# Kernel optimization log

Hardware: AMD Instinct MI355X
Metric: run time of the kernel (lower is better)

Reference implementation:

```python
import jax, jax.numpy as jnp
import numpy as np

NUM_HEADS = 12


def setup_inputs() -> dict:
    key = jax.random.key(0)
    k_x, k_m, k_qkv, k_proj = jax.random.split(key, 4)
    B, N, C = 2, 2048, 768
    x = jax.random.normal(k_x, (B, N, C), dtype=jnp.float32)
    # binary key mask: 1 = attend, 0 = masked out
    mask = jax.random.randint(k_m, (B, N), 0, 2).astype(jnp.int32)
    # torch Linear(dim, dim*3, bias=False): stored here as [in, out]
    w_qkv = jax.random.normal(k_qkv, (C, 3 * C), dtype=jnp.float32) * 0.02
    w_proj = jax.random.normal(k_proj, (C, C), dtype=jnp.float32) * 0.02
    b_proj = jnp.zeros((C,), dtype=jnp.float32)
    return {"x": x, "mask": mask, "w_qkv": w_qkv, "w_proj": w_proj, "b_proj": b_proj}


def reference(x, mask, w_qkv, w_proj, b_proj):
    B, N, C = x.shape
    H = NUM_HEADS
    hd = C // H
    scale = hd ** -0.5
    qkv = (x @ w_qkv).reshape(B, N, 3, H, hd)
    q, k, v = jnp.moveaxis(qkv, 2, 0)            # each [B, N, H, hd]
    attn = jnp.einsum('bnhd,bmhd->bhnm', q, k) * scale  # [B, H, N, N]
    # faithful masked_softmax: unstable exp (no max subtraction), mask keys, renormalize
    m = mask.astype(x.dtype)[:, None, None, :]   # [B, 1, 1, N]
    x_exp = jnp.exp(attn) * m
    attn = x_exp / x_exp.sum(-1, keepdims=True)
    out = jnp.einsum('bhnm,bmhd->bnhd', attn, v).reshape(B, N, C)
    return out @ w_proj + b_proj
```

## Files before the change

kernel.cpp:

```cpp
#include <hip/hip_runtime.h>
#include <cstdint>

#define NB 2
#define NSEQ 2048
#define CDIM 768
#define NH 12
#define HD 64
#define NTOK (NB*NSEQ)
#define QKV_COLS (3*CDIM)
#define NBLK ((NSEQ/64)*NH*NB)

typedef short bf16x8 __attribute__((ext_vector_type(8)));
typedef short bf16x4 __attribute__((ext_vector_type(4)));
typedef float f32x4  __attribute__((ext_vector_type(4)));
typedef short short4v __attribute__((ext_vector_type(4)));
typedef unsigned int uint4v __attribute__((ext_vector_type(4)));

#define MFMA16(a,b,c) __builtin_amdgcn_mfma_f32_16x16x32_bf16(a,b,c,0,0,0)

__device__ __forceinline__ short f2b(float f) {
    uint32_t u = __builtin_bit_cast(uint32_t, f);
    u += 0x7fffu + ((u >> 16) & 1u);
    return (short)(u >> 16);
}
__device__ __forceinline__ unsigned pack2(float a, float b) {
    unsigned ua = __builtin_bit_cast(unsigned, a) + 0x7fffu;
    unsigned ub = __builtin_bit_cast(unsigned, b) + 0x7fffu;
    return __builtin_amdgcn_perm(ub, ua, 0x07060302u);
}
__device__ __forceinline__ void gll16(const short* g, short* l) {
    __builtin_amdgcn_global_load_lds(
        (const __attribute__((address_space(1))) unsigned int*)g,
        (__attribute__((address_space(3))) unsigned int*)l, 16, 0, 0);
}

__global__ __launch_bounds__(256) void prep_kernel(
    const float* __restrict__ x, const float* __restrict__ w_qkv,
    const float* __restrict__ w_proj,
    short* __restrict__ xb, short* __restrict__ wqt, short* __restrict__ wpt)
{
    __shared__ float tile[32][33];
    const int bid = blockIdx.x, t = threadIdx.x;
    if (bid < 3072) {
        int i = bid * 256 + t;
        float4 v = ((const float4*)x)[i];
        short4v o = { f2b(v.x), f2b(v.y), f2b(v.z), f2b(v.w) };
        ((short4v*)xb)[i] = o;
        return;
    }
    const float* w; short* wt; int K, NC, n0, k0;
    if (bid < 3072 + 1728) {
        int r = bid - 3072;
        w = w_qkv; wt = wqt; K = CDIM; NC = QKV_COLS;
        n0 = (r % 72) * 32; k0 = (r / 72) * 32;
    } else {
        int r = bid - 4800;
        w = w_proj; wt = wpt; K = CDIM; NC = CDIM;
        n0 = (r % 24) * 32; k0 = (r / 24) * 32;
    }
    #pragma unroll
    for (int i = 0; i < 4; ++i) {
        int idx = t + i * 256; int r = idx >> 5, c = idx & 31;
        tile[r][c] = w[(size_t)(k0 + r) * NC + n0 + c];
    }
    __syncthreads();
    #pragma unroll
    for (int i = 0; i < 4; ++i) {
        int idx = t + i * 256; int r = idx >> 5, c = idx & 31;
        wt[(size_t)(n0 + r) * K + k0 + c] = f2b(tile[c][r]);
    }
}

__global__ __launch_bounds__(256) void gemm_qkv(
    const short* __restrict__ A ,
    const short* __restrict__ B ,
    short* __restrict__ qb, short* __restrict__ kb, short* __restrict__ vt)
{
    __shared__ short As[128 * 32];
    __shared__ short Bs[128 * 32];
    const int t = threadIdx.x;
    const int lane = t & 63, wid = t >> 6;
    const int quad = lane >> 4, l16 = lane & 15;
    const int wA = wid >> 1, wB = wid & 1;
    const int n0 = blockIdx.x * 128;
    const int m0 = blockIdx.y * 128;

    const int srow = wid * 16 + (lane >> 2), schunk = (lane & 3) * 8;
    const short* ag0 = A + (size_t)(n0 + srow) * CDIM + schunk;
    const short* ag1 = ag0 + (size_t)64 * CDIM;
    const short* bg0 = B + (size_t)(m0 + srow) * CDIM + schunk;
    const short* bg1 = bg0 + (size_t)64 * CDIM;
    short* asl0 = &As[(wid * 16) * 32];
    short* asl1 = &As[(wid * 16 + 64) * 32];
    short* bsl0 = &Bs[(wid * 16) * 32];
    short* bsl1 = &Bs[(wid * 16 + 64) * 32];

    f32x4 acc[4][4] = {};
    for (int k0 = 0; k0 < CDIM; k0 += 32) {
        __syncthreads();
        gll16(ag0 + k0, asl0);
        gll16(ag1 + k0, asl1);
        gll16(bg0 + k0, bsl0);
        gll16(bg1 + k0, bsl1);
        __syncthreads();
        bf16x8 af[4], bf[4];
        #pragma unroll
        for (int i = 0; i < 4; ++i)
            af[i] = *(const bf16x8*)&As[(wA*64 + i*16 + l16) * 32 + quad*8];
        #pragma unroll
        for (int j = 0; j < 4; ++j)
            bf[j] = *(const bf16x8*)&Bs[(wB*64 + j*16 + l16) * 32 + quad*8];
        #pragma unroll
        for (int i = 0; i < 4; ++i)
            #pragma unroll
            for (int j = 0; j < 4; ++j)
                acc[i][j] = MFMA16(af[i], bf[j], acc[i][j]);
    }

    const int colbase = n0 + wA * 64;
    const int s = colbase / CDIM;
    const int h = (colbase - s * CDIM) >> 6;
    const int b = m0 >> 11;
    const size_t bh = (size_t)(b * NH + h);
    const float qsc = (s == 0) ? 0.125f : 1.0f;
    #pragma unroll
    for (int i = 0; i < 4; ++i) {
        const int d0 = i*16 + quad*4;
        #pragma unroll
        for (int j = 0; j < 4; ++j) {
            int tok = (m0 + wB*64 + j*16 + l16) & (NSEQ - 1);
            if (s < 2) {
                short* dst = (s == 0 ? qb : kb) + (bh * NSEQ + tok) * HD + d0;
                short4v o = { f2b(acc[i][j][0] * qsc), f2b(acc[i][j][1] * qsc),
                              f2b(acc[i][j][2] * qsc), f2b(acc[i][j][3] * qsc) };
                *(short4v*)dst = o;
            } else {
                short* dst = vt + (bh * HD + d0) * NSEQ + tok;
                #pragma unroll
                for (int r = 0; r < 4; ++r)
                    dst[(size_t)r * NSEQ] = f2b(acc[i][j][r]);
            }
        }
    }
}

#define STAGE(KT, BUF) do {                                                      \
    short* kb_ = (BUF);                                                          \
    short* vb_ = (BUF) + 8192;                                                   \
    _Pragma("unroll")                                                            \
    for (int j = 0; j < 4; ++j) {                                                \
        gll16(kp + (size_t)((KT) + rK[j]) * HD + cK[j]*8,                        \
              kb_ + wid*2048 + j*512);                                           \
        gll16(vp + (size_t)dV[j] * NSEQ + (KT) + cV[j]*8,                        \
              vb_ + wid*2048 + j*512);                                           \
    }                                                                            \
} while (0)

#define BODY(KT, BUF) do {                                                       \
    const short* KsB_ = (BUF);                                                   \
    const short* VsB_ = (BUF) + 8192;                                            \
    int4 mi0_ = *(const int4*)(mp + (KT) + kbase);                               \
    int4 mi1_ = *(const int4*)(mp + (KT) + 64 + kbase);                          \
    bf16x8 kf00_ = *(const bf16x8*)&KsB_[krow + kc0];                            \
    bf16x8 kf01_ = *(const bf16x8*)&KsB_[krow + kc1];                            \
    bf16x8 kf10_ = *(const bf16x8*)&KsB_[4096 + krow + kc0];                     \
    bf16x8 kf11_ = *(const bf16x8*)&KsB_[4096 + krow + kc1];                     \
    f32x4 s0_[4] = {}, s1_[4] = {};                                              \
    _Pragma("unroll")                                                            \
    for (int jt = 0; jt < 4; ++jt) {                                             \
        s0_[jt] = MFMA16(kf00_, qf[jt][0], s0_[jt]);                             \
        s0_[jt] = MFMA16(kf01_, qf[jt][1], s0_[jt]);                             \
        s1_[jt] = MFMA16(kf10_, qf[jt][0], s1_[jt]);                             \
        s1_[jt] = MFMA16(kf11_, qf[jt][1], s1_[jt]);                             \
    }                                                                            \
    float4 m0_ = {(float)mi0_.x, (float)mi0_.y, (float)mi0_.z, (float)mi0_.w};   \
    float4 m1_ = {(float)mi1_.x, (float)mi1_.y, (float)mi1_.z, (float)mi1_.w};   \
    bf16x8 pb_[4];                                                               \
    _Pragma("unroll")                                                            \
    for (int jt = 0; jt < 4; ++jt) {                                             \
        float e0 = __expf(s0_[jt][0]) * m0_.x;                                   \
        float e1 = __expf(s0_[jt][1]) * m0_.y;                                   \
        float e2 = __expf(s0_[jt][2]) * m0_.z;                                   \
        float e3 = __expf(s0_[jt][3]) * m0_.w;                                   \
        float f0 = __expf(s1_[jt][0]) * m1_.x;                                   \
        float f1 = __expf(s1_[jt][1]) * m1_.y;                                   \
        float f2 = __expf(s1_[jt][2]) * m1_.z;                                   \
        float f3 = __expf(s1_[jt][3]) * m1_.w;                                   \
        l[jt] += ((e0 + e1) + (e2 + e3)) + ((f0 + f1) + (f2 + f3));              \
        uint4v pk_ = { pack2(e0, e1), pack2(e2, e3),                             \
                       pack2(f0, f1), pack2(f2, f3) };                           \
        pb_[jt] = __builtin_bit_cast(bf16x8, pk_);                               \
    }                                                                            \
    _Pragma("unroll")                                                            \
    for (int it = 0; it < 4; ++it) {                                             \
        const int vrow_ = (it*16 + l16) * 128;                                   \
        bf16x4 lo_ = *(const bf16x4*)&VsB_[vrow_ + vposl + vsub];                \
        bf16x4 hi_ = *(const bf16x4*)&VsB_[vrow_ + vposh + vsub];                \
        bf16x8 vf_ = __builtin_shufflevector(lo_, hi_, 0,1,2,3,4,5,6,7);         \
        _Pragma("unroll")                                                        \
        for (int jt = 0; jt < 4; ++jt)                                           \
            o_acc[it][jt] = MFMA16(vf_, pb_[jt], o_acc[it][jt]);                 \
    }                                                                            \
} while (0)

__global__ __launch_bounds__(256, 2) void attn_kernel(
    const short* __restrict__ qb, const short* __restrict__ kb,
    const short* __restrict__ vt, const int* __restrict__ mask,
    short* __restrict__ ao)
{
    __shared__ __align__(16) short KV[2][16384];
    float (*Ob)[68] = (float(*)[68])KV;
    float (*lsum)[64] = (float(*)[64])((char*)KV + 17408);

    const int t = threadIdx.x;
    const int lane = t & 63, wid = t >> 6;
    const int quad = lane >> 4, l16 = lane & 15;
    const int id = blockIdx.x;
    const int idx = id >> 3;
    const int bh = (id & 7) + ((idx % 3) << 3);
    const int q0 = (idx / 3) << 6;
    const int b = bh / NH, h = bh - b * NH;
    const size_t hoff = (size_t)bh * NSEQ * HD;
    const short* qp = qb + hoff;
    const short* kp = kb + hoff;
    const short* vp = vt + hoff;
    const int* mp = mask + b * NSEQ;
    const int kbase = wid * 16 + quad * 4;

    int rK[4], cK[4], dV[4], cV[4];
    #pragma unroll
    for (int j = 0; j < 4; ++j) {
        int o = wid * 4096 + j * 1024 + lane * 16;
        rK[j] = o >> 7;
        cK[j] = ((o >> 4) & 7) ^ (rK[j] & 7);
        dV[j] = o >> 8;
        cV[j] = ((o >> 4) & 15) ^ (dV[j] & 15);
    }
    const int r7 = l16 & 7;
    const int krow = (wid * 16 + l16) * 64;
    const int kc0 = ((quad     ^ r7) << 3);
    const int kc1 = (((quad+4) ^ r7) << 3);
    const int vposl = ((wid*2 + (quad >> 1)) ^ l16) << 3;
    const int vposh = (((8 + wid*2 + (quad >> 1)) ^ l16) << 3);
    const int vsub = (quad & 1) * 4;

    bf16x8 qf[4][2];
    #pragma unroll
    for (int jt = 0; jt < 4; ++jt) {
        const short* qr = qp + (size_t)(q0 + jt*16 + l16) * HD + quad*8;
        qf[jt][0] = *(const bf16x8*)qr;
        qf[jt][1] = *(const bf16x8*)(qr + 32);
    }

    f32x4 o_acc[4][4] = {};
    float l[4] = {0.f, 0.f, 0.f, 0.f};

    STAGE(0, KV[0]);
    __syncthreads();

    for (int kt = 0; kt < NSEQ; kt += 256) {
        STAGE(kt + 128, KV[1]);
        BODY(kt, KV[0]);
        __syncthreads();
        const int nx = (kt + 256) & (NSEQ - 1);
        STAGE(nx, KV[0]);
        BODY(kt + 128, KV[1]);
        __syncthreads();
    }

    #pragma unroll
    for (int jt = 0; jt < 4; ++jt) {
        l[jt] += __shfl_xor(l[jt], 16);
        l[jt] += __shfl_xor(l[jt], 32);
        if (quad == 0) lsum[wid][jt*16 + l16] = l[jt];
    }
    for (int w = 0; w < 4; ++w) {
        __syncthreads();
        if (wid == w) {
            #pragma unroll
            for (int it = 0; it < 4; ++it)
                #pragma unroll
                for (int jt = 0; jt < 4; ++jt)
                    #pragma unroll
                    for (int r = 0; r < 4; ++r) {
                        if (w == 0)
                            Ob[it*16 + quad*4 + r][jt*16 + l16] = o_acc[it][jt][r];
                        else
                            Ob[it*16 + quad*4 + r][jt*16 + l16] += o_acc[it][jt][r];
                    }
        }
    }
    __syncthreads();

    {
        const int ql = t >> 2, dc = (t & 3) * 16;
        float inv = 1.0f / (((lsum[0][ql] + lsum[1][ql]) +
                             (lsum[2][ql] + lsum[3][ql])));
        bf16x8 o8a, o8b;
        #pragma unroll
        for (int d = 0; d < 8; ++d) o8a[d] = f2b(Ob[dc + d][ql] * inv);
        #pragma unroll
        for (int d = 0; d < 8; ++d) o8b[d] = f2b(Ob[dc + 8 + d][ql] * inv);
        int tok = b * NSEQ + q0 + ql;
        short* dst = ao + (size_t)tok * CDIM + h * HD + dc;
        *(bf16x8*)dst = o8a;
        *(bf16x8*)(dst + 8) = o8b;
    }
}

__global__ __launch_bounds__(256) void gemm_proj(
    const short* __restrict__ A ,
    const short* __restrict__ B ,
    const float* __restrict__ bias, float* __restrict__ out)
{
    __shared__ short As[128 * 32];
    __shared__ short Bs[128 * 32];
    const int t = threadIdx.x;
    const int lane = t & 63, wid = t >> 6;
    const int quad = lane >> 4, l16 = lane & 15;
    const int wA = wid >> 1, wB = wid & 1;
    const int n0 = blockIdx.x * 128;
    const int m0 = blockIdx.y * 128;

    const int srow = wid * 16 + (lane >> 2), schunk = (lane & 3) * 8;
    const short* ag0 = A + (size_t)(n0 + srow) * CDIM + schunk;
    const short* ag1 = ag0 + (size_t)64 * CDIM;
    const short* bg0 = B + (size_t)(m0 + srow) * CDIM + schunk;
    const short* bg1 = bg0 + (size_t)64 * CDIM;
    short* asl0 = &As[(wid * 16) * 32];
    short* asl1 = &As[(wid * 16 + 64) * 32];
    short* bsl0 = &Bs[(wid * 16) * 32];
    short* bsl1 = &Bs[(wid * 16 + 64) * 32];

    f32x4 acc[4][4] = {};
    for (int k0 = 0; k0 < CDIM; k0 += 32) {
        __syncthreads();
        gll16(ag0 + k0, asl0);
        gll16(ag1 + k0, asl1);
        gll16(bg0 + k0, bsl0);
        gll16(bg1 + k0, bsl1);
        __syncthreads();
        bf16x8 af[4], bf[4];
        #pragma unroll
        for (int i = 0; i < 4; ++i)
            af[i] = *(const bf16x8*)&As[(wA*64 + i*16 + l16) * 32 + quad*8];
        #pragma unroll
        for (int j = 0; j < 4; ++j)
            bf[j] = *(const bf16x8*)&Bs[(wB*64 + j*16 + l16) * 32 + quad*8];
        #pragma unroll
        for (int i = 0; i < 4; ++i)
            #pragma unroll
            for (int j = 0; j < 4; ++j)
                acc[i][j] = MFMA16(af[i], bf[j], acc[i][j]);
    }

    #pragma unroll
    for (int i = 0; i < 4; ++i) {
        int col0 = n0 + wA*64 + i*16 + quad*4;
        float4 bias4 = *(const float4*)&bias[col0];
        #pragma unroll
        for (int j = 0; j < 4; ++j) {
            int tok = m0 + wB*64 + j*16 + l16;
            float4 o = { acc[i][j][0] + bias4.x, acc[i][j][1] + bias4.y,
                         acc[i][j][2] + bias4.z, acc[i][j][3] + bias4.w };
            *(float4*)(out + (size_t)tok * CDIM + col0) = o;
        }
    }
}

extern "C" void kernel_launch(void* const* d_in, const int* in_sizes, int n_in,
                              void* d_out, int out_size, void* d_ws, size_t ws_size,
                              hipStream_t stream)
{
    const float* x      = (const float*)d_in[0];
    const int*   mask   = (const int*)d_in[1];
    const float* w_qkv  = (const float*)d_in[2];
    const float* w_proj = (const float*)d_in[3];
    const float* b_proj = (const float*)d_in[4];
    float* out = (float*)d_out;

    const size_t SZ = (size_t)NTOK * CDIM;
    short* xb  = (short*)d_ws;
    short* wqt = xb  + SZ;
    short* wpt = wqt + (size_t)QKV_COLS * CDIM;
    short* qb  = wpt + (size_t)CDIM * CDIM;
    short* kb  = qb  + SZ;
    short* vt  = kb  + SZ;
    short* ao  = vt  + SZ;

    dim3 blk(256);
    prep_kernel<<<dim3(5376), blk, 0, stream>>>(x, w_qkv, w_proj, xb, wqt, wpt);
    gemm_qkv<<<dim3(QKV_COLS/128, NTOK/128), blk, 0, stream>>>(wqt, xb, qb, kb, vt);
    attn_kernel<<<dim3(NBLK), blk, 0, stream>>>(qb, kb, vt, mask, ao);
    gemm_proj<<<dim3(CDIM/128, NTOK/128), blk, 0, stream>>>(wpt, ao, b_proj, out);
}
```

Measured before the change: 177.0 us.

## Double-buffer GEMM LDS tiles and halve N tile to 64 for more blocks

Both projection GEMMs now use a two-stage LDS ping-pong, so the next K slice is loaded while MFMAs run on the current one. The old loop had two barriers per K step and no load/compute overlap. The output tile also shrinks from 128x128 to 64x128, doubling the grid (notably gemm_proj goes from 192 to 384 blocks) to fill more CUs. The cost is less reuse of each loaded tile and more total global traffic; the loop also issues one redundant prefetch at the end.

Result: slower. 184.1 us (+4.0%).

```diff
diff --git a/kernel.cpp b/kernel.cpp
--- a/kernel.cpp
+++ b/kernel.cpp
@@ -71,68 +71,77 @@
     }
 }
 
+#define GSTAGE(K0, BUF) do {                                                     \
+    gll16(ag + (K0), As + (BUF)*4096 + wid*512);                                 \
+    gll16(bg0 + (K0), Bs + (BUF)*8192 + wid*1024);                               \
+    gll16(bg1 + (K0), Bs + (BUF)*8192 + wid*1024 + 512);                         \
+} while (0)
+
+#define GCOMP(BUF) do {                                                          \
+    const short* A_ = As + (BUF)*4096;                                           \
+    const short* B_ = Bs + (BUF)*8192;                                           \
+    bf16x8 af_[2], bf_[4];                                                       \
+    _Pragma("unroll")                                                            \
+    for (int i = 0; i < 2; ++i)                                                  \
+        af_[i] = *(const bf16x8*)&A_[(wA*32 + i*16 + l16) * 32 + quad*8];        \
+    _Pragma("unroll")                                                            \
+    for (int j = 0; j < 4; ++j)                                                  \
+        bf_[j] = *(const bf16x8*)&B_[(wB*64 + j*16 + l16) * 32 + quad*8];        \
+    _Pragma("unroll")                                                            \
+    for (int i = 0; i < 2; ++i)                                                  \
+        _Pragma("unroll")                                                        \
+        for (int j = 0; j < 4; ++j)                                              \
+            acc[i][j] = MFMA16(af_[i], bf_[j], acc[i][j]);                       \
+} while (0)
+
+#define GEMM_LOOP() do {                                                         \
+    GSTAGE(0, 0); __syncthreads();                                               \
+    for (int k0 = 0; k0 < CDIM; k0 += 64) {                                      \
+        GSTAGE(k0 + 32, 1);                                                      \
+        GCOMP(0);                                                                \
+        __syncthreads();                                                         \
+        GSTAGE((k0 + 64 < CDIM) ? k0 + 64 : 0, 0);                               \
+        GCOMP(1);                                                                \
+        __syncthreads();                                                         \
+    }                                                                            \
+} while (0)
+
 __global__ __launch_bounds__(256) void gemm_qkv(
     const short* __restrict__ A ,
     const short* __restrict__ B ,
     short* __restrict__ qb, short* __restrict__ kb, short* __restrict__ vt)
 {
-    __shared__ short As[128 * 32];
-    __shared__ short Bs[128 * 32];
+    __shared__ __align__(16) short As[8192];
+    __shared__ __align__(16) short Bs[16384];
     const int t = threadIdx.x;
     const int lane = t & 63, wid = t >> 6;
     const int quad = lane >> 4, l16 = lane & 15;
     const int wA = wid >> 1, wB = wid & 1;
-    const int n0 = blockIdx.x * 128;
+    const int n0 = blockIdx.x * 64;
     const int m0 = blockIdx.y * 128;
 
-    const int srow = wid * 16 + (lane >> 2), schunk = (lane & 3) * 8;
-    const short* ag0 = A + (size_t)(n0 + srow) * CDIM + schunk;
-    const short* ag1 = ag0 + (size_t)64 * CDIM;
-    const short* bg0 = B + (size_t)(m0 + srow) * CDIM + schunk;
-    const short* bg1 = bg0 + (size_t)64 * CDIM;
-    short* asl0 = &As[(wid * 16) * 32];
-    short* asl1 = &As[(wid * 16 + 64) * 32];
-    short* bsl0 = &Bs[(wid * 16) * 32];
-    short* bsl1 = &Bs[(wid * 16 + 64) * 32];
-
-    f32x4 acc[4][4] = {};
-    for (int k0 = 0; k0 < CDIM; k0 += 32) {
-        __syncthreads();
-        gll16(ag0 + k0, asl0);
-        gll16(ag1 + k0, asl1);
-        gll16(bg0 + k0, bsl0);
-        gll16(bg1 + k0, bsl1);
-        __syncthreads();
-        bf16x8 af[4], bf[4];
-        #pragma unroll
-        for (int i = 0; i < 4; ++i)
-            af[i] = *(const bf16x8*)&As[(wA*64 + i*16 + l16) * 32 + quad*8];
-        #pragma unroll
-        for (int j = 0; j < 4; ++j)
-            bf[j] = *(const bf16x8*)&Bs[(wB*64 + j*16 + l16) * 32 + quad*8];
-        #pragma unroll
-        for (int i = 0; i < 4; ++i)
-            #pragma unroll
-            for (int j = 0; j < 4; ++j)
-                acc[i][j] = MFMA16(af[i], bf[j], acc[i][j]);
-    }
-
-    const int colbase = n0 + wA * 64;
-    const int s = colbase / CDIM;
-    const int h = (colbase - s * CDIM) >> 6;
+    const short* ag  = A + (size_t)(n0 + wid*16 + (lane >> 2)) * CDIM + (lane & 3)*8;
+    const short* bg0 = B + (size_t)(m0 + wid*32 + (lane >> 2)) * CDIM + (lane & 3)*8;
+    const short* bg1 = bg0 + (size_t)16 * CDIM;
+
+    f32x4 acc[2][4] = {};
+    GEMM_LOOP();
+
+    const int s = n0 / CDIM;
+    const int h = (n0 - s * CDIM) >> 6;
     const int b = m0 >> 11;
     const size_t bh = (size_t)(b * NH + h);
     const float qsc = (s == 0) ? 0.125f : 1.0f;
     #pragma unroll
-    for (int i = 0; i < 4; ++i) {
-        const int d0 = i*16 + quad*4;
+    for (int i = 0; i < 2; ++i) {
+        const int d0 = wA*32 + i*16 + quad*4;
         #pragma unroll
         for (int j = 0; j < 4; ++j) {
-            int tok = (m0 + wB*64 + j*16 + l16) & (NSEQ - 1);
+            int tok = (m0 & (NSEQ - 1)) + wB*64 + j*16 + l16;
             if (s < 2) {
                 short* dst = (s == 0 ? qb : kb) + (bh * NSEQ + tok) * HD + d0;
-                short4v o = { f2b(acc[i][j][0] * qsc), f2b(acc[i][j][1] * qsc),
-                              f2b(acc[i][j][2] * qsc), f2b(acc[i][j][3] * qsc) };
+                short4v o = { f2b(acc[i][j][0]*qsc), f2b(acc[i][j][1]*qsc),
+                              f2b(acc[i][j][2]*qsc), f2b(acc[i][j][3]*qsc) };
                 *(short4v*)dst = o;
             } else {
                 short* dst = vt + (bh * HD + d0) * NSEQ + tok;
@@ -313,50 +322,25 @@
     const short* __restrict__ B ,
     const float* __restrict__ bias, float* __restrict__ out)
 {
-    __shared__ short As[128 * 32];
-    __shared__ short Bs[128 * 32];
+    __shared__ __align__(16) short As[8192];
+    __shared__ __align__(16) short Bs[16384];
     const int t = threadIdx.x;
     const int lane = t & 63, wid = t >> 6;
     const int quad = lane >> 4, l16 = lane & 15;
     const int wA = wid >> 1, wB = wid & 1;
-    const int n0 = blockIdx.x * 128;
+    const int n0 = blockIdx.x * 64;
     const int m0 = blockIdx.y * 128;
 
-    const int srow = wid * 16 + (lane >> 2), schunk = (lane & 3) * 8;
-    const short* ag0 = A + (size_t)(n0 + srow) * CDIM + schunk;
-    const short* ag1 = ag0 + (size_t)64 * CDIM;
-    const short* bg0 = B + (size_t)(m0 + srow) * CDIM + schunk;
-    const short* bg1 = bg0 + (size_t)64 * CDIM;
-    short* asl0 = &As[(wid * 16) * 32];
-    short* asl1 = &As[(wid * 16 + 64) * 32];
-    short* bsl0 = &Bs[(wid * 16) * 32];
-    short* bsl1 = &Bs[(wid * 16 + 64) * 32];
-
-    f32x4 acc[4][4] = {};
-    for (int k0 = 0; k0 < CDIM; k0 += 32) {
-        __syncthreads();
-        gll16(ag0 + k0, asl0);
-        gll16(ag1 + k0, asl1);
-        gll16(bg0 + k0, bsl0);
-        gll16(bg1 + k0, bsl1);
-        __syncthreads();
-        bf16x8 af[4], bf[4];
-        #pragma unroll
-        for (int i = 0; i < 4; ++i)
-            af[i] = *(const bf16x8*)&As[(wA*64 + i*16 + l16) * 32 + quad*8];
-        #pragma unroll
-        for (int j = 0; j < 4; ++j)
-            bf[j] = *(const bf16x8*)&Bs[(wB*64 + j*16 + l16) * 32 + quad*8];
-        #pragma unroll
-        for (int i = 0; i < 4; ++i)
-            #pragma unroll
-            for (int j = 0; j < 4; ++j)
-                acc[i][j] = MFMA16(af[i], bf[j], acc[i][j]);
-    }
-
-    #pragma unroll
-    for (int i = 0; i < 4; ++i) {
-        int col0 = n0 + wA*64 + i*16 + quad*4;
+    const short* ag  = A + (size_t)(n0 + wid*16 + (lane >> 2)) * CDIM + (lane & 3)*8;
+    const short* bg0 = B + (size_t)(m0 + wid*32 + (lane >> 2)) * CDIM + (lane & 3)*8;
+    const short* bg1 = bg0 + (size_t)16 * CDIM;
+
+    f32x4 acc[2][4] = {};
+    GEMM_LOOP();
+
+    #pragma unroll
+    for (int i = 0; i < 2; ++i) {
+        int col0 = n0 + wA*32 + i*16 + quad*4;
         float4 bias4 = *(const float4*)&bias[col0];
         #pragma unroll
         for (int j = 0; j < 4; ++j) {
@@ -390,7 +374,7 @@
 
     dim3 blk(256);
     prep_kernel<<<dim3(5376), blk, 0, stream>>>(x, w_qkv, w_proj, xb, wqt, wpt);
-    gemm_qkv<<<dim3(QKV_COLS/128, NTOK/128), blk, 0, stream>>>(wqt, xb, qb, kb, vt);
+    gemm_qkv<<<dim3(QKV_COLS/64, NTOK/128), blk, 0, stream>>>(wqt, xb, qb, kb, vt);
     attn_kernel<<<dim3(NBLK), blk, 0, stream>>>(qb, kb, vt, mask, ao);
-    gemm_proj<<<dim3(CDIM/128, NTOK/128), blk, 0, stream>>>(wpt, ao, b_proj, out);
-}
+    gemm_proj<<<dim3(CDIM/64, NTOK/128), blk, 0, stream>>>(wpt, ao, b_proj, out);
+}
```
